# Performance work log

Hardware: AMD Instinct MI355X
Metric: run time of the kernel (lower is better)

Reference implementation:

```python
import jax, jax.numpy as jnp
import numpy as np

LN_EPS = 1e-5   # torch LayerNorm default
NRM_EPS = 1e-8  # normalizer-state epsilon in mLSTMCell


def setup_inputs() -> dict:
    key = jax.random.key(0)
    ks = jax.random.split(key, 3)
    B, T, H, L, O = 32, 256, 1024, 4, 256
    x = jax.random.normal(ks[0], (B, T, H), dtype=jnp.float32)
    # 6 projections per layer in order (q, k, v, i, f, o); Linear stored as [in, out]
    W = jax.random.normal(ks[1], (L, 6, H, H), dtype=jnp.float32) * 0.02
    b = jnp.zeros((L, 6, H), dtype=jnp.float32)
    ln_g = jnp.ones((L, 6, H), dtype=jnp.float32)
    ln_b = jnp.zeros((L, 6, H), dtype=jnp.float32)
    fc_w = jax.random.normal(ks[2], (H, O), dtype=jnp.float32) * 0.02
    fc_b = jnp.zeros((O,), dtype=jnp.float32)
    return {"x": x, "W": W, "b": b, "ln_g": ln_g, "ln_b": ln_b,
            "fc_w": fc_w, "fc_b": fc_b}


def _layer_norm(z, g, beta):
    # z: [6, B, H]; g, beta: [6, H]
    mu = z.mean(-1, keepdims=True)
    var = z.var(-1, keepdims=True)
    return (z - mu) * jax.lax.rsqrt(var + LN_EPS) * g[:, None, :] + beta[:, None, :]


def _cell(x_in, h_prev, c_prev, n_prev, Wl, bl, gl, betal):
    # x_in: [B, H]; states: [B, H]; Wl: [6, H, H]
    z = jnp.einsum('bh,jhd->jbd', x_in, Wl) + bl[:, None, :]
    z = _layer_norm(z, gl, betal)
    q, k, v, zi, zf, zo = z  # q is computed by the original cell but unused
    i = jnp.exp(zi)
    f = jax.nn.sigmoid(zf)
    o = jax.nn.sigmoid(zo)
    # kv_interaction = outer(k, v); sum over dim=1 == sum(k) * v (same math, no [B,H,H])
    kv_sum = k.sum(-1, keepdims=True) * v
    c = f * c_prev + i * kv_sum
    n = f * n_prev + i * k
    n_hat = n / (jnp.linalg.norm(n, axis=-1, keepdims=True) + NRM_EPS)
    h = o * jnp.tanh(c * n_hat)
    return h, c, n


def _mlstm_forward(x, W, b, ln_g, ln_b, fc_w, fc_b):
    B, T, H = x.shape
    L = W.shape[0]
    h0 = jnp.zeros((L, B, H), x.dtype)
    init = (h0, h0, h0)  # (h, c, n)

    def step(carry, x_t):
        h, c, n = carry
        layer_in = x_t
        hs, cs, ns = [], [], []
        for l in range(L):  # small fixed layer count
            h_l, c_l, n_l = _cell(layer_in, h[l], c[l], n[l],
                                  W[l], b[l], ln_g[l], ln_b[l])
            if l > 0:  # residual connection (use_residual=True)
                h_l = h_l + layer_in
            layer_in = h_l
            hs.append(h_l); cs.append(c_l); ns.append(n_l)
        return (jnp.stack(hs), jnp.stack(cs), jnp.stack(ns)), None

    (h, c, n), _ = jax.lax.scan(step, init, jnp.swapaxes(x, 0, 1))
    # output[-1] == top-layer hidden at the final timestep
    out = h[-1] @ fc_w + fc_b  # [B, O]
    return out, (h, c, n)


def reference(x, W, b, ln_g, ln_b, fc_w, fc_b):
    return _mlstm_forward(x, W, b, ln_g, ln_b, fc_w, fc_b)
```

## Files before the change

kernel.cpp:

```cpp
#include <hip/hip_runtime.h>
#include <hip/hip_bf16.h>
#include <math.h>

#define H 1024
#define B 32
#define T 256
#define L 4
#define O 256
#define TCH 128
#define NCHUNK 2
#define SEGLEN 16
#define NSEG (TCH / SEGLEN)

typedef _Float16 half8 __attribute__((ext_vector_type(8)));
typedef _Float16 half4 __attribute__((ext_vector_type(4)));
typedef float f32x4 __attribute__((ext_vector_type(4)));

#define X_PK_OFF   0
#define HB0_OFF    8388608
#define HB1_OFF    16777216
#define WT2_OFF    25165824
#define Z16_OFF    46137344
#define A_OFF      67108864
#define BC_OFF     75497472
#define BN_OFF     83886080
#define STATS_OFF  92274688
#define CARC_OFF   92372992
#define CARN_OFF   92897280
#define STATE_OFF  93421568
#define FCP_OFF    93945856

__global__ __launch_bounds__(256) void pack_w(const float* __restrict__ W,
                                              _Float16* __restrict__ Wt2) {
  int tile = blockIdx.x;
  int m_idx = tile >> 8;
  int kt = (tile >> 4) & 15, ntt = tile & 15;
  int l = m_idx / 5, jj = m_idx % 5;
  const float* Wf = W + ((size_t)(l * 6 + jj + 1) << 20);
  _Float16* out = Wt2 + ((size_t)m_idx << 20);
  __shared__ float ts[64][65];
  int k0 = kt * 64, n0 = ntt * 64;
#pragma unroll
  for (int s = 0; s < 16; ++s) {
    int e = threadIdx.x + s * 256;
    int kk = e >> 6, col = e & 63;
    ts[kk][col] = Wf[(size_t)(k0 + kk) * H + n0 + col];
  }
  __syncthreads();
#pragma unroll
  for (int gi = 0; gi < 2; ++gi) {
    int g = threadIdx.x * 2 + gi;
    int l64 = g & 63, ksl = (g >> 6) & 1, ntl = g >> 7;
    int nn = l64 & 15, kh = l64 >> 4;
    half8 tmp;
#pragma unroll
    for (int e = 0; e < 8; ++e)
      tmp[e] = (_Float16)ts[ksl * 32 + kh * 8 + e][ntl * 16 + nn];
    *(half8*)&out[(size_t)((ntt * 4 + ntl) * 32 + kt * 2 + ksl) * 512 + (size_t)l64 * 8] = tmp;
  }
}

__global__ __launch_bounds__(256) void pack_x(const float* __restrict__ x,
                                              _Float16* __restrict__ x_pk) {
  int t = blockIdx.x;
  __shared__ float ld[32][257];
  for (int c = 0; c < 4; ++c) {
#pragma unroll
    for (int s = 0; s < 32; ++s) {
      int e2 = threadIdx.x + s * 256;
      int b = e2 >> 8, col = e2 & 255;
      ld[b][col] = x[((size_t)b * T + t) * H + c * 256 + col];
    }
    __syncthreads();
#pragma unroll
    for (int s3 = 0; s3 < 4; ++s3) {
      int gg = threadIdx.x * 4 + s3;
      int l64 = gg & 63, ksl = (gg >> 6) & 7, bt = gg >> 9;
      int nn = l64 & 15, kh = l64 >> 4;
      int b = bt * 16 + nn;
      half8 tmp;
#pragma unroll
      for (int e = 0; e < 8; ++e)
        tmp[e] = (_Float16)ld[b][ksl * 32 + kh * 8 + e];
      *(half8*)&x_pk[(size_t)t * 32768 + (size_t)bt * 16384 +
                     (size_t)(c * 8 + ksl) * 512 + (size_t)l64 * 8] = tmp;
    }
    __syncthreads();
  }
}

__global__ __launch_bounds__(512) void gemm_big(
    const _Float16* __restrict__ A_pk, const _Float16* __restrict__ Wl,
    _Float16* __restrict__ z16, int t0) {
  int raw = blockIdx.x;
  int swz = (raw & 7) * 80 + (raw >> 3);
  int bm = swz & 31;
  int bn = swz >> 5;
  int w = threadIdx.x >> 6, lane = threadIdx.x & 63;
  int wm = w >> 2, wn = w & 3;

  __shared__ _Float16 smem[24576];

  int j = bn >> 2;
  const _Float16* gsrc[3];
  int ldst[3];
#pragma unroll
  for (int q = 0; q < 3; ++q) {
    int f = w * 3 + q;
    if (f < 8) {
      gsrc[q] = A_pk + (size_t)(t0 * 2 + bm * 8 + f) * 16384 + lane * 8;
      ldst[q] = f * 512 + lane * 8;
    } else {
      int nf = f - 8;
      gsrc[q] = Wl + ((size_t)j << 20) + (size_t)((bn & 3) * 16 + nf) * 16384 + lane * 8;
      ldst[q] = 4096 + nf * 512 + lane * 8;
    }
  }

  half8 stA[3], stB[3];
#pragma unroll
  for (int q = 0; q < 3; ++q) stA[q] = *(const half8*)(gsrc[q]);
#pragma unroll
  for (int q = 0; q < 3; ++q) *(half8*)&smem[ldst[q]] = stA[q];
#pragma unroll
  for (int q = 0; q < 3; ++q) stA[q] = *(const half8*)(gsrc[q] + 512);
  __syncthreads();

  f32x4 acc[4][4] = {};
  int ardo = wm * 2048 + lane * 8;
  int brdo = 4096 + wn * 2048 + lane * 8;

  for (int ks = 0; ks < 32; ks += 2) {
    {
      if (ks + 2 < 32) {
#pragma unroll
        for (int q = 0; q < 3; ++q)
          stB[q] = *(const half8*)(gsrc[q] + (size_t)(ks + 2) * 512);
      }
      half8 a[4], b[4];
#pragma unroll
      for (int i = 0; i < 4; ++i) a[i] = *(const half8*)&smem[ardo + i * 512];
#pragma unroll
      for (int i = 0; i < 4; ++i) b[i] = *(const half8*)&smem[brdo + i * 512];
#pragma unroll
      for (int i = 0; i < 4; ++i)
#pragma unroll
        for (int jf = 0; jf < 4; ++jf)
          acc[i][jf] = __builtin_amdgcn_mfma_f32_16x16x32_f16(a[i], b[jf], acc[i][jf], 0, 0, 0);
#pragma unroll
      for (int q = 0; q < 3; ++q) *(half8*)&smem[12288 + ldst[q]] = stA[q];
      asm volatile("s_waitcnt lgkmcnt(0)" ::: "memory");
      __builtin_amdgcn_s_barrier();
      __builtin_amdgcn_sched_barrier(0);
    }
    {
      if (ks + 3 < 32) {
#pragma unroll
        for (int q = 0; q < 3; ++q)
          stA[q] = *(const half8*)(gsrc[q] + (size_t)(ks + 3) * 512);
      }
      half8 a[4], b[4];
#pragma unroll
      for (int i = 0; i < 4; ++i) a[i] = *(const half8*)&smem[12288 + ardo + i * 512];
#pragma unroll
      for (int i = 0; i < 4; ++i) b[i] = *(const half8*)&smem[12288 + brdo + i * 512];
#pragma unroll
      for (int i = 0; i < 4; ++i)
#pragma unroll
        for (int jf = 0; jf < 4; ++jf)
          acc[i][jf] = __builtin_amdgcn_mfma_f32_16x16x32_f16(a[i], b[jf], acc[i][jf], 0, 0, 0);
      if (ks + 2 < 32) {
#pragma unroll
        for (int q = 0; q < 3; ++q) *(half8*)&smem[ldst[q]] = stB[q];
        asm volatile("s_waitcnt lgkmcnt(0)" ::: "memory");
        __builtin_amdgcn_s_barrier();
        __builtin_amdgcn_sched_barrier(0);
      }
    }
  }
  __syncthreads();

  _Float16 (*cz)[264] = (_Float16(*)[264])smem;
  int hb0 = (bn & 3) * 256;
  for (int p = 0; p < 2; ++p) {
    if (p) __syncthreads();
    if (wm == p) {
#pragma unroll
      for (int i = 0; i < 4; ++i)
#pragma unroll
        for (int jf = 0; jf < 4; ++jf)
#pragma unroll
          for (int r = 0; r < 4; ++r)
            cz[i * 16 + (lane >> 4) * 4 + r][wn * 64 + jf * 16 + (lane & 15)] =
                (_Float16)acc[i][jf][r];
    }
    __syncthreads();
#pragma unroll
    for (int s = 0; s < 4; ++s) {
      int e = threadIdx.x + s * 512;
      int r = e >> 5, h8 = e & 31;
      int m_local = bm * 128 + p * 64 + r;
      half8 vv = *(const half8*)&cz[r][h8 * 8];
      *(half8*)&z16[((size_t)m_local * 5 + j) * 1024 + hb0 + h8 * 8] = vv;
    }
  }
}

__global__ __launch_bounds__(256) void stats_kernel(
    const _Float16* __restrict__ z16, const float* __restrict__ bias,
    const float* __restrict__ ln_g, const float* __restrict__ ln_b,
    float* __restrict__ stats, int l) {
  int row = blockIdx.x, tid = threadIdx.x;
  int h0 = tid * 4;
  float red[13];
#pragma unroll
  for (int jj = 0; jj < 5; ++jj) {
    half4 z4 = *(const half4*)&z16[((size_t)row * 5 + jj) * 1024 + h0];
    float4 bb = *(const float4*)&bias[(size_t)(l * 6 + 1 + jj) * H + h0];
    float vx = (float)z4[0] + bb.x, vy = (float)z4[1] + bb.y,
          vz = (float)z4[2] + bb.z, vw = (float)z4[3] + bb.w;
    red[jj * 2] = vx + vy + vz + vw;
    red[jj * 2 + 1] = vx * vx + vy * vy + vz * vz + vw * vw;
    if (jj == 0) {
      float4 g = *(const float4*)&ln_g[(size_t)(l * 6 + 1) * H + h0];
      float4 be = *(const float4*)&ln_b[(size_t)(l * 6 + 1) * H + h0];
      red[10] = vx * g.x + vy * g.y + vz * g.z + vw * g.w;
      red[11] = g.x + g.y + g.z + g.w;
      red[12] = be.x + be.y + be.z + be.w;
    }
  }
#pragma unroll
  for (int off = 32; off; off >>= 1)
#pragma unroll
    for (int q = 0; q < 13; ++q) red[q] += __shfl_down(red[q], off);
  __shared__ float sb[4][13];
  if ((tid & 63) == 0) {
#pragma unroll
    for (int q = 0; q < 13; ++q) sb[tid >> 6][q] = red[q];
  }
  __syncthreads();
  if (tid == 0) {
    float st[13];
#pragma unroll
    for (int q = 0; q < 13; ++q) st[q] = sb[0][q] + sb[1][q] + sb[2][q] + sb[3][q];
    float* so = stats + (size_t)row * 12;
#pragma unroll
    for (int jj = 0; jj < 5; ++jj) {
      float mu = st[jj * 2] * (1.0f / H);
      float var = st[jj * 2 + 1] * (1.0f / H) - mu * mu;
      so[jj * 2] = mu;
      so[jj * 2 + 1] = rsqrtf(var + 1e-5f);
    }
    float mu0 = st[0] * (1.0f / H);
    float rs0 = rsqrtf(st[1] * (1.0f / H) - mu0 * mu0 + 1e-5f);
    so[10] = rs0 * (st[10] - mu0 * st[11]) + st[12];
    so[11] = 0.f;
  }
}

__global__ __launch_bounds__(256) void scan_p1(
    const _Float16* __restrict__ z16, const float* __restrict__ stats,
    const float* __restrict__ bias, const float* __restrict__ ln_g,
    const float* __restrict__ ln_b, float* __restrict__ Abuf,
    float* __restrict__ Bc, float* __restrict__ Bn, int l) {
  int idx = blockIdx.x * 256 + threadIdx.x;
  int h = idx & 1023;
  int bs = idx >> 10;
  int b = bs & 31, seg = bs >> 5;

  float bz[4], gg[4], bb[4];
#pragma unroll
  for (int jj = 0; jj < 4; ++jj) {
    bz[jj] = bias[(size_t)(l * 6 + 1 + jj) * H + h];
    gg[jj] = ln_g[(size_t)(l * 6 + 1 + jj) * H + h];
    bb[jj] = ln_b[(size_t)(l * 6 + 1 + jj) * H + h];
  }
  float A = 1.f, bc = 0.f, bn = 0.f;
#pragma unroll 2
  for (int u = 0; u < SEGLEN; ++u) {
    int row = (seg * SEGLEN + u) * 32 + b;
    size_t zb = ((size_t)row * 5) * 1024 + h;
    float zk = (float)z16[zb];
    float zv = (float)z16[zb + 1024];
    float zi = (float)z16[zb + 2048];
    float zf = (float)z16[zb + 3072];
    const float* st = stats + (size_t)row * 12;
    float k   = (zk + bz[0] - st[0]) * st[1] * gg[0] + bb[0];
    float v   = (zv + bz[1] - st[2]) * st[3] * gg[1] + bb[1];
    float zi_ = (zi + bz[2] - st[4]) * st[5] * gg[2] + bb[2];
    float zf_ = (zf + bz[3] - st[6]) * st[7] * gg[3] + bb[3];
    float iv = __expf(zi_);
    float fv = 1.f / (1.f + __expf(-zf_));
    A *= fv;
    bn = fv * bn + iv * k;
    bc = fv * bc + iv * (st[10] * v);
    size_t o = (size_t)row * 1024 + h;
    Abuf[o] = A;
    Bn[o] = bn;
    Bc[o] = bc;
  }
}

__global__ __launch_bounds__(256) void scan_p2(
    const float* __restrict__ Abuf, const float* __restrict__ Bc,
    const float* __restrict__ Bn, float* __restrict__ state,
    float* __restrict__ carC, float* __restrict__ carN, int l, int t0) {
  int idx = blockIdx.x * 256 + threadIdx.x;
  int h = idx & 1023, b = idx >> 10;
  size_t sidx = ((size_t)l * B + b) * H + h;
  float cc = 0.f, nn = 0.f;
  if (t0 > 0) {
    cc = state[sidx];
    nn = state[(size_t)L * B * H + sidx];
  }
#pragma unroll
  for (int seg = 0; seg < NSEG; ++seg) {
    size_t coff = (size_t)seg * 32768 + (size_t)b * 1024 + h;
    carC[coff] = cc;
    carN[coff] = nn;
    int rowLast = (seg * SEGLEN + SEGLEN - 1) * 32 + b;
    size_t o = (size_t)rowLast * 1024 + h;
    float a = Abuf[o];
    cc = Bc[o] + a * cc;
    nn = Bn[o] + a * nn;
  }
  state[sidx] = cc;
  state[(size_t)L * B * H + sidx] = nn;
}

__global__ __launch_bounds__(256) void final_kernel(
    const _Float16* __restrict__ z16, const float* __restrict__ stats,
    const float* __restrict__ bias, const float* __restrict__ ln_g,
    const float* __restrict__ ln_b, const float* __restrict__ Abuf,
    const float* __restrict__ Bc, const float* __restrict__ Bn,
    const float* __restrict__ carC, const float* __restrict__ carN,
    const _Float16* __restrict__ hin, _Float16* __restrict__ hout,
    float* __restrict__ out, int l, int t0) {
  int row = blockIdx.x;
  int b = row & 31, tc = row >> 5, t = t0 + tc, seg = tc / SEGLEN;
  int tid = threadIdx.x, h0 = tid * 4;
  size_t o = (size_t)row * 1024 + h0;
  size_t coff = (size_t)seg * 32768 + (size_t)b * 1024 + h0;
  float4 a4 = *(const float4*)&Abuf[o];
  float4 bn4 = *(const float4*)&Bn[o];
  float4 bc4 = *(const float4*)&Bc[o];
  float4 cN = *(const float4*)&carN[coff];
  float4 cC = *(const float4*)&carC[coff];
  float nn[4] = {bn4.x + a4.x * cN.x, bn4.y + a4.y * cN.y,
                 bn4.z + a4.z * cN.z, bn4.w + a4.w * cN.w};
  float cc[4] = {bc4.x + a4.x * cC.x, bc4.y + a4.y * cC.y,
                 bc4.z + a4.z * cC.z, bc4.w + a4.w * cC.w};

  float ss = nn[0] * nn[0] + nn[1] * nn[1] + nn[2] * nn[2] + nn[3] * nn[3];
#pragma unroll
  for (int off = 32; off; off >>= 1) ss += __shfl_down(ss, off);
  __shared__ float sb[4];
  if ((tid & 63) == 0) sb[tid >> 6] = ss;
  __syncthreads();
  float rn = 1.f / (sqrtf(sb[0] + sb[1] + sb[2] + sb[3]) + 1e-8f);

  half4 zo4 = *(const half4*)&z16[((size_t)row * 5 + 4) * 1024 + h0];
  const float* st = stats + (size_t)row * 12;
  float mu = st[8], rs = st[9];
  float4 bz = *(const float4*)&bias[(size_t)(l * 6 + 5) * H + h0];
  float4 g4 = *(const float4*)&ln_g[(size_t)(l * 6 + 5) * H + h0];
  float4 be4 = *(const float4*)&ln_b[(size_t)(l * 6 + 5) * H + h0];
  float gv[4] = {g4.x, g4.y, g4.z, g4.w};
  float bev[4] = {be4.x, be4.y, be4.z, be4.w};
  float zov[4] = {(float)zo4[0] + bz.x, (float)zo4[1] + bz.y,
                  (float)zo4[2] + bz.z, (float)zo4[3] + bz.w};

  size_t hfoff = (size_t)(b >> 4) * 16384 + (size_t)(h0 >> 5) * 512 +
                 (size_t)((((h0 & 31) >> 3) * 16) + (b & 15)) * 8 + (h0 & 7);
  half4 rin;
  if (l > 0) rin = *(const half4*)&hin[(size_t)t * 32768 + hfoff];

  float hh[4];
#pragma unroll
  for (int u = 0; u < 4; ++u) {
    float ov = 1.f / (1.f + __expf(-((zov[u] - mu) * rs * gv[u] + bev[u])));
    float targ = cc[u] * (nn[u] * rn);
    float e2 = __expf(-2.f * fabsf(targ));
    float th = copysignf((1.f - e2) / (1.f + e2), targ);
    hh[u] = ov * th + ((l > 0) ? (float)rin[u] : 0.f);
  }
  half4 hx;
  hx[0] = (_Float16)hh[0]; hx[1] = (_Float16)hh[1];
  hx[2] = (_Float16)hh[2]; hx[3] = (_Float16)hh[3];
  *(half4*)&hout[(size_t)t * 32768 + hfoff] = hx;

  if (t == T - 1) {
    *(float4*)&out[8192 + (size_t)l * 32768 + (size_t)b * 1024 + h0] =
        make_float4(hh[0], hh[1], hh[2], hh[3]);
    *(float4*)&out[8192 + 131072 + ((size_t)(l * B) + b) * 1024 + h0] =
        make_float4(cc[0], cc[1], cc[2], cc[3]);
    *(float4*)&out[8192 + 262144 + ((size_t)(l * B) + b) * 1024 + h0] =
        make_float4(nn[0], nn[1], nn[2], nn[3]);
  }
}

__global__ __launch_bounds__(256) void fc_part(
    const float* __restrict__ out_h, const float* __restrict__ fc_w,
    float* __restrict__ partial) {
  int b = blockIdx.x >> 3, kh = blockIdx.x & 7;
  int o = threadIdx.x;
  const float* hr = out_h + (size_t)b * 1024 + kh * 128;
  const float* wp = fc_w + (size_t)kh * 128 * O + o;
  float acc = 0.f;
#pragma unroll 8
  for (int h = 0; h < 128; ++h)
    acc = fmaf(hr[h], wp[(size_t)h * O], acc);
  partial[((size_t)kh * 32 + b) * O + o] = acc;
}

__global__ __launch_bounds__(256) void fc_reduce(
    const float* __restrict__ partial, const float* __restrict__ fc_b,
    float* __restrict__ out) {
  int b = blockIdx.x, o = threadIdx.x;
  float acc = fc_b[o];
#pragma unroll
  for (int kh = 0; kh < 8; ++kh)
    acc += partial[((size_t)kh * 32 + b) * O + o];
  out[(size_t)b * O + o] = acc;
}

extern "C" void kernel_launch(void* const* d_in, const int* in_sizes, int n_in,
                              void* d_out, int out_size, void* d_ws, size_t ws_size,
                              hipStream_t stream) {
  const float* x    = (const float*)d_in[0];
  const float* W    = (const float*)d_in[1];
  const float* bias = (const float*)d_in[2];
  const float* ln_g = (const float*)d_in[3];
  const float* ln_b = (const float*)d_in[4];
  const float* fc_w = (const float*)d_in[5];
  const float* fc_b = (const float*)d_in[6];
  float* out = (float*)d_out;
  _Float16* wsh = (_Float16*)d_ws;

  _Float16* x_pk = wsh + X_PK_OFF;
  _Float16* hb[2] = {wsh + HB0_OFF, wsh + HB1_OFF};
  _Float16* Wt2  = wsh + WT2_OFF;
  _Float16* z16  = wsh + Z16_OFF;
  float* Abuf  = (float*)(wsh + A_OFF);
  float* Bc    = (float*)(wsh + BC_OFF);
  float* Bn    = (float*)(wsh + BN_OFF);
  float* stats = (float*)(wsh + STATS_OFF);
  float* carC  = (float*)(wsh + CARC_OFF);
  float* carN  = (float*)(wsh + CARN_OFF);
  float* state = (float*)(wsh + STATE_OFF);
  float* fcp   = (float*)(wsh + FCP_OFF);

  pack_w<<<5120, 256, 0, stream>>>(W, Wt2);
  pack_x<<<256, 256, 0, stream>>>(x, x_pk);

  for (int l = 0; l < L; ++l) {
    const _Float16* A_in = (l == 0) ? x_pk : hb[(l - 1) & 1];
    _Float16* h_out = hb[l & 1];
    const _Float16* Wl = Wt2 + ((size_t)(l * 5) << 20);
    for (int c = 0; c < NCHUNK; ++c) {
      int t0 = c * TCH;
      gemm_big<<<640, 512, 0, stream>>>(A_in, Wl, z16, t0);
      stats_kernel<<<4096, 256, 0, stream>>>(z16, bias, ln_g, ln_b, stats, l);
      scan_p1<<<1024, 256, 0, stream>>>(z16, stats, bias, ln_g, ln_b,
                                        Abuf, Bc, Bn, l);
      scan_p2<<<128, 256, 0, stream>>>(Abuf, Bc, Bn, state, carC, carN, l, t0);
      final_kernel<<<4096, 256, 0, stream>>>(z16, stats, bias, ln_g, ln_b,
                                             Abuf, Bc, Bn, carC, carN,
                                             A_in, h_out, out, l, t0);
    }
  }
  fc_part<<<256, 256, 0, stream>>>(out + 8192 + 3 * 32768, fc_w, fcp);
  fc_reduce<<<B, 256, 0, stream>>>(fcp, fc_b, out);
}
```

Baseline: 893.9 us.

## Process the full sequence per layer instead of two time chunks

Removes the two-chunk time split, so each layer launches one GEMM, stats, scan and final pass over all 256 timesteps with doubled grid sizes. The cross-chunk state carry through global memory goes away and the kernel launch count per layer is halved. The GEMM block swizzle is remapped so each XCD handles a contiguous block of M and N tiles. In exchange the workspace grows, since z16 and the scan buffers now hold the whole sequence, and the serial scan_p2 loop now runs twice as many segments.

```diff
diff --git a/kernel.cpp b/kernel.cpp
--- a/kernel.cpp
+++ b/kernel.cpp
@@ -7,10 +7,8 @@
 #define T 256
 #define L 4
 #define O 256
-#define TCH 128
-#define NCHUNK 2
 #define SEGLEN 16
-#define NSEG (TCH / SEGLEN)
+#define NSEG (T / SEGLEN)
 
 typedef _Float16 half8 __attribute__((ext_vector_type(8)));
 typedef _Float16 half4 __attribute__((ext_vector_type(4)));
@@ -21,14 +19,14 @@
 #define HB1_OFF    16777216
 #define WT2_OFF    25165824
 #define Z16_OFF    46137344
-#define A_OFF      67108864
-#define BC_OFF     75497472
-#define BN_OFF     83886080
-#define STATS_OFF  92274688
-#define CARC_OFF   92372992
-#define CARN_OFF   92897280
-#define STATE_OFF  93421568
-#define FCP_OFF    93945856
+#define A_OFF      88080384
+#define BC_OFF     104857600
+#define BN_OFF     121634816
+#define STATS_OFF  138412032
+#define CARC_OFF   138608640
+#define CARN_OFF   139657216
+#define STATE_OFF  140705792
+#define FCP_OFF    141230080
 
 __global__ __launch_bounds__(256) void pack_w(const float* __restrict__ W,
                                               _Float16* __restrict__ Wt2) {
@@ -91,11 +89,11 @@
 
 __global__ __launch_bounds__(512) void gemm_big(
     const _Float16* __restrict__ A_pk, const _Float16* __restrict__ Wl,
-    _Float16* __restrict__ z16, int t0) {
+    _Float16* __restrict__ z16) {
   int raw = blockIdx.x;
-  int swz = (raw & 7) * 80 + (raw >> 3);
-  int bm = swz & 31;
-  int bn = swz >> 5;
+  int xcd = raw & 7, c = raw >> 3;
+  int bm = (xcd >> 1) * 16 + (c & 15);
+  int bn = (xcd & 1) * 10 + (c >> 4);
   int w = threadIdx.x >> 6, lane = threadIdx.x & 63;
   int wm = w >> 2, wn = w & 3;
 
@@ -108,7 +106,7 @@
   for (int q = 0; q < 3; ++q) {
     int f = w * 3 + q;
     if (f < 8) {
-      gsrc[q] = A_pk + (size_t)(t0 * 2 + bm * 8 + f) * 16384 + lane * 8;
+      gsrc[q] = A_pk + (size_t)(bm * 8 + f) * 16384 + lane * 8;
       ldst[q] = f * 512 + lane * 8;
     } else {
       int nf = f - 8;
@@ -303,16 +301,11 @@
 
 __global__ __launch_bounds__(256) void scan_p2(
     const float* __restrict__ Abuf, const float* __restrict__ Bc,
-    const float* __restrict__ Bn, float* __restrict__ state,
-    float* __restrict__ carC, float* __restrict__ carN, int l, int t0) {
+    const float* __restrict__ Bn, float* __restrict__ carC,
+    float* __restrict__ carN) {
   int idx = blockIdx.x * 256 + threadIdx.x;
   int h = idx & 1023, b = idx >> 10;
-  size_t sidx = ((size_t)l * B + b) * H + h;
   float cc = 0.f, nn = 0.f;
-  if (t0 > 0) {
-    cc = state[sidx];
-    nn = state[(size_t)L * B * H + sidx];
-  }
 #pragma unroll
   for (int seg = 0; seg < NSEG; ++seg) {
     size_t coff = (size_t)seg * 32768 + (size_t)b * 1024 + h;
@@ -324,8 +317,6 @@
     cc = Bc[o] + a * cc;
     nn = Bn[o] + a * nn;
   }
-  state[sidx] = cc;
-  state[(size_t)L * B * H + sidx] = nn;
 }
 
 __global__ __launch_bounds__(256) void final_kernel(
@@ -335,9 +326,9 @@
     const float* __restrict__ Bc, const float* __restrict__ Bn,
     const float* __restrict__ carC, const float* __restrict__ carN,
     const _Float16* __restrict__ hin, _Float16* __restrict__ hout,
-    float* __restrict__ out, int l, int t0) {
+    float* __restrict__ out, int l) {
   int row = blockIdx.x;
-  int b = row & 31, tc = row >> 5, t = t0 + tc, seg = tc / SEGLEN;
+  int b = row & 31, t = row >> 5, seg = t / SEGLEN;
   int tid = threadIdx.x, h0 = tid * 4;
   size_t o = (size_t)row * 1024 + h0;
   size_t coff = (size_t)seg * 32768 + (size_t)b * 1024 + h0;
@@ -447,7 +438,6 @@
   float* stats = (float*)(wsh + STATS_OFF);
   float* carC  = (float*)(wsh + CARC_OFF);
   float* carN  = (float*)(wsh + CARN_OFF);
-  float* state = (float*)(wsh + STATE_OFF);
   float* fcp   = (float*)(wsh + FCP_OFF);
 
   pack_w<<<5120, 256, 0, stream>>>(W, Wt2);
@@ -457,17 +447,14 @@
     const _Float16* A_in = (l == 0) ? x_pk : hb[(l - 1) & 1];
     _Float16* h_out = hb[l & 1];
     const _Float16* Wl = Wt2 + ((size_t)(l * 5) << 20);
-    for (int c = 0; c < NCHUNK; ++c) {
-      int t0 = c * TCH;
-      gemm_big<<<640, 512, 0, stream>>>(A_in, Wl, z16, t0);
-      stats_kernel<<<4096, 256, 0, stream>>>(z16, bias, ln_g, ln_b, stats, l);
-      scan_p1<<<1024, 256, 0, stream>>>(z16, stats, bias, ln_g, ln_b,
-                                        Abuf, Bc, Bn, l);
-      scan_p2<<<128, 256, 0, stream>>>(Abuf, Bc, Bn, state, carC, carN, l, t0);
-      final_kernel<<<4096, 256, 0, stream>>>(z16, stats, bias, ln_g, ln_b,
-                                             Abuf, Bc, Bn, carC, carN,
-                                             A_in, h_out, out, l, t0);
-    }
+    gemm_big<<<1280, 512, 0, stream>>>(A_in, Wl, z16);
+    stats_kernel<<<8192, 256, 0, stream>>>(z16, bias, ln_g, ln_b, stats, l);
+    scan_p1<<<2048, 256, 0, stream>>>(z16, stats, bias, ln_g, ln_b,
+                                      Abuf, Bc, Bn, l);
+    scan_p2<<<128, 256, 0, stream>>>(Abuf, Bc, Bn, carC, carN);
+    final_kernel<<<8192, 256, 0, stream>>>(z16, stats, bias, ln_g, ln_b,
+                                           Abuf, Bc, Bn, carC, carN,
+                                           A_in, h_out, out, l);
   }
   fc_part<<<256, 256, 0, stream>>>(out + 8192 + 3 * 32768, fc_w, fcp);
   fc_reduce<<<B, 256, 0, stream>>>(fcp, fc_b, out);
```

Result: faster. 793.6 us (-11.2%).
